# Performance work log

Measured on AMD Instinct MI355X. Metric: run time of the kernel, lower is better.

The kernel has to match this reference:

```python
import jax, jax.numpy as jnp
import numpy as np

D_MODEL = 1024
NHEAD = 16
D_K = D_MODEL // NHEAD


def setup_inputs() -> dict:
    key = jax.random.key(0)
    ks = jax.random.split(key, 8)
    B, S = 2, 2048
    scale = 1.0 / np.sqrt(D_MODEL)
    return {
        "Q": jax.random.normal(ks[0], (B, S, D_MODEL), dtype=jnp.float32),
        "K": jax.random.normal(ks[1], (B, S, D_MODEL), dtype=jnp.float32),
        "V": jax.random.normal(ks[2], (B, S, D_MODEL), dtype=jnp.float32),
        "WQ": jax.random.normal(ks[3], (D_MODEL, D_MODEL), dtype=jnp.float32) * scale,
        "WK": jax.random.normal(ks[4], (D_MODEL, D_MODEL), dtype=jnp.float32) * scale,
        "WV": jax.random.normal(ks[5], (D_MODEL, D_MODEL), dtype=jnp.float32) * scale,
        "Wfc": jax.random.normal(ks[6], (D_MODEL, D_MODEL), dtype=jnp.float32) * scale,
        "bfc": jax.random.normal(ks[7], (D_MODEL,), dtype=jnp.float32) * 0.01,
    }


def reference(Q, K, V, WQ, WK, WV, Wfc, bfc):
    B, Sq, _ = Q.shape
    Skv = K.shape[1]
    # Linear projections (torch Linear: x @ W^T), split into heads: [B, H, S, d_k]
    q = (Q @ WQ.T).reshape(B, Sq, NHEAD, D_K).transpose(0, 2, 1, 3)
    k = (K @ WK.T).reshape(B, Skv, NHEAD, D_K).transpose(0, 2, 1, 3)
    v = (V @ WV.T).reshape(B, Skv, NHEAD, D_K).transpose(0, 2, 1, 3)
    # Scaled dot-product scores: [B, H, Sq, Skv]
    scores = jnp.einsum("bhqd,bhkd->bhqk", q, k) / jnp.sqrt(jnp.float32(D_K))
    # Causal mask (strict upper triangle -> -inf)
    causal = jnp.tril(jnp.ones((Sq, Skv), dtype=bool))
    scores = jnp.where(causal, scores, -jnp.inf)
    attn = jax.nn.softmax(scores, axis=-1)
    y = jnp.einsum("bhqk,bhkd->bhqd", attn, v)
    y = y.transpose(0, 2, 1, 3).reshape(B, Sq, D_MODEL)
    return y @ Wfc.T + bfc
```

## Files before the change

kernel.cpp:

```cpp
#include <hip/hip_runtime.h>

typedef __attribute__((ext_vector_type(8))) short bf16x8;
typedef __attribute__((ext_vector_type(4))) float f32x4;
typedef __attribute__((ext_vector_type(16))) float f32x16;

__device__ __forceinline__ ushort f2bf(float f) {
    union { float f; unsigned u; } x; x.f = f;
    unsigned r = x.u + 0x7fffu + ((x.u >> 16) & 1u);
    return (ushort)(r >> 16);
}

__device__ __forceinline__ void async16(const void* g, void* l) {
    __builtin_amdgcn_global_load_lds(
        (const __attribute__((address_space(1))) void*)g,
        (__attribute__((address_space(3))) void*)l, 16, 0, 0);
}

__device__ __forceinline__ f32x4 mfma16(bf16x8 a, bf16x8 b, f32x4 c) {
    return __builtin_amdgcn_mfma_f32_16x16x32_bf16(a, b, c, 0, 0, 0);
}
__device__ __forceinline__ f32x16 mfma32(bf16x8 a, bf16x8 b, f32x16 c) {
    return __builtin_amdgcn_mfma_f32_32x32x16_bf16(a, b, c, 0, 0, 0);
}

__device__ __forceinline__ f32x4 zero4() { f32x4 z = {0.f, 0.f, 0.f, 0.f}; return z; }

#define PIPE_BARRIER(cond_more)                                          \
    do {                                                                 \
        if (cond_more) asm volatile("s_waitcnt vmcnt(4)" ::: "memory");  \
        else           asm volatile("s_waitcnt vmcnt(0)" ::: "memory");  \
        asm volatile("s_waitcnt lgkmcnt(0)" ::: "memory");               \
        __builtin_amdgcn_sched_barrier(0);                               \
        __builtin_amdgcn_s_barrier();                                    \
        __builtin_amdgcn_sched_barrier(0);                               \
    } while (0)

__global__ void cvt7_kernel(
    const float* __restrict__ s0, const float* __restrict__ s1, const float* __restrict__ s2,
    const float* __restrict__ s3, const float* __restrict__ s4, const float* __restrict__ s5,
    const float* __restrict__ s6,
    ushort* __restrict__ d0, ushort* __restrict__ d1, ushort* __restrict__ d2,
    ushort* __restrict__ d3, ushort* __restrict__ d4, ushort* __restrict__ d5,
    ushort* __restrict__ d6)
{
    int y = blockIdx.y;
    const float* s; ushort* d; int n4;
    if      (y == 0) { s = s0; d = d0; n4 = 1048576; }
    else if (y == 1) { s = s1; d = d1; n4 = 1048576; }
    else if (y == 2) { s = s2; d = d2; n4 = 1048576; }
    else if (y == 3) { s = s3; d = d3; n4 = 262144; }
    else if (y == 4) { s = s4; d = d4; n4 = 262144; }
    else if (y == 5) { s = s5; d = d5; n4 = 262144; }
    else             { s = s6; d = d6; n4 = 262144; }
    int i = blockIdx.x * 256 + threadIdx.x;
    if (i >= n4) return;
    float4 v = ((const float4*)s)[i];
    ushort4 o;
    o.x = f2bf(v.x); o.y = f2bf(v.y); o.z = f2bf(v.z); o.w = f2bf(v.w);
    ((ushort4*)d)[i] = o;
}

template<bool SWAP>
__device__ __forceinline__ void gemm_core(
    const ushort* __restrict__ A, const ushort* __restrict__ W,
    char* smem, int bm, int bn, int tid, f32x4 acc[4][4])
{
    const int lane = tid & 63;
    const int wid  = tid >> 6;
    const int wr = wid >> 1, wc = wid & 1;
    const int l15 = lane & 15, g = lane >> 4;

    auto stage = [&](int kt) {
        char* As = smem + (kt % 3) * 16384;
        char* Bs = As + 8192;
        #pragma unroll
        for (int it = 0; it < 2; ++it) {
            int c = it * 256 + tid;
            int row = c >> 2, inner = c & 3;
            int srcoff = (inner ^ (row & 3)) * 16;
            async16((const char*)A + (size_t)(bm * 128 + row) * 2048 + kt * 64 + srcoff, As + c * 16);
            async16((const char*)W + (size_t)(bn * 128 + row) * 2048 + kt * 64 + srcoff, Bs + c * 16);
        }
    };

    stage(0);
    stage(1);

    for (int kt = 0; kt < 32; ++kt) {
        PIPE_BARRIER(kt < 31);
        if (kt < 30) stage(kt + 2);

        const char* As = smem + (kt % 3) * 16384;
        const char* Bs = As + 8192;
        bf16x8 af[4], bfr[4];
        #pragma unroll
        for (int mt = 0; mt < 4; ++mt) {
            int row = wr * 64 + mt * 16 + l15;
            af[mt] = *(const bf16x8*)(As + ((row * 64 + g * 16) ^ ((row & 3) << 4)));
        }
        #pragma unroll
        for (int nt = 0; nt < 4; ++nt) {
            int row = wc * 64 + nt * 16 + l15;
            bfr[nt] = *(const bf16x8*)(Bs + ((row * 64 + g * 16) ^ ((row & 3) << 4)));
        }
        __builtin_amdgcn_s_setprio(1);
        #pragma unroll
        for (int mt = 0; mt < 4; ++mt)
            #pragma unroll
            for (int nt = 0; nt < 4; ++nt) {
                if (SWAP) acc[mt][nt] = mfma16(bfr[nt], af[mt], acc[mt][nt]);
                else      acc[mt][nt] = mfma16(af[mt], bfr[nt], acc[mt][nt]);
            }
        __builtin_amdgcn_s_setprio(0);
    }
}

__global__ __launch_bounds__(256, 2) void gemm_qkv(
    const ushort* __restrict__ Qb, const ushort* __restrict__ Kb, const ushort* __restrict__ Vb,
    const ushort* __restrict__ WQ, const ushort* __restrict__ WK, const ushort* __restrict__ WV,
    ushort* __restrict__ qhb, ushort* __restrict__ khb, ushort* __restrict__ vhT)
{
    __shared__ __align__(16) char smem[49152];
    const int tid = threadIdx.x;
    const int z  = blockIdx.x % 3;
    const int bm = blockIdx.x / 3;
    const int bn = blockIdx.y;
    const int lane = tid & 63;
    const int wid  = tid >> 6;
    const int wr = wid >> 1, wc = wid & 1;
    const int l15 = lane & 15, g = lane >> 4;

    const ushort* A  = (z == 0) ? Qb : (z == 1) ? Kb : Vb;
    const ushort* Wm = (z == 0) ? WQ : (z == 1) ? WK : WV;

    f32x4 acc[4][4];
    #pragma unroll
    for (int i = 0; i < 4; ++i)
        #pragma unroll
        for (int j = 0; j < 4; ++j) acc[i][j] = zero4();

    if (z == 2) {
        gemm_core<true>(A, Wm, smem, bm, bn, tid, acc);
        #pragma unroll
        for (int mt = 0; mt < 4; ++mt)
            #pragma unroll
            for (int nt = 0; nt < 4; ++nt)
                #pragma unroll
                for (int j = 0; j < 4; ++j) {
                    int n = bn * 128 + wc * 64 + nt * 16 + g * 4 + j;
                    int m = bm * 128 + wr * 64 + mt * 16 + l15;
                    int b = m >> 11, s = m & 2047, h = (n >> 6) & 15, d = n & 63;
                    vhT[(((size_t)(b * 16 + h)) * 64 + d) * 2048 + s] = f2bf(acc[mt][nt][j]);
                }
    } else {
        gemm_core<false>(A, Wm, smem, bm, bn, tid, acc);
        const float scale = (z == 0) ? 0.125f : 1.0f;
        ushort* outb = (z == 0) ? qhb : khb;
        #pragma unroll
        for (int mt = 0; mt < 4; ++mt)
            #pragma unroll
            for (int nt = 0; nt < 4; ++nt)
                #pragma unroll
                for (int j = 0; j < 4; ++j) {
                    int m = bm * 128 + wr * 64 + mt * 16 + g * 4 + j;
                    int n = bn * 128 + wc * 64 + nt * 16 + l15;
                    int b = m >> 11, s = m & 2047, h = n >> 6, d = n & 63;
                    outb[(((size_t)(b * 16 + h)) * 2048 + s) * 64 + d] = f2bf(acc[mt][nt][j] * scale);
                }
    }
}

__global__ __launch_bounds__(256, 2) void gemm_fc(
    const ushort* __restrict__ A, const ushort* __restrict__ W,
    float* __restrict__ outf, const float* __restrict__ bias)
{
    __shared__ __align__(16) char smem[49152];
    const int tid = threadIdx.x;
    const int lane = tid & 63;
    const int wid  = tid >> 6;
    const int wr = wid >> 1, wc = wid & 1;
    const int l15 = lane & 15, g = lane >> 4;

    f32x4 acc[4][4];
    #pragma unroll
    for (int i = 0; i < 4; ++i)
        #pragma unroll
        for (int j = 0; j < 4; ++j) acc[i][j] = zero4();

    gemm_core<false>(A, W, smem, blockIdx.x, blockIdx.y, tid, acc);

    #pragma unroll
    for (int mt = 0; mt < 4; ++mt)
        #pragma unroll
        for (int nt = 0; nt < 4; ++nt)
            #pragma unroll
            for (int j = 0; j < 4; ++j) {
                int m = blockIdx.x * 128 + wr * 64 + mt * 16 + g * 4 + j;
                int n = blockIdx.y * 128 + wc * 64 + nt * 16 + l15;
                outf[(size_t)m * 1024 + n] = acc[mt][nt][j] + bias[n];
            }
}

__global__ __launch_bounds__(512, 2) void attn_kernel(
    const ushort* __restrict__ qh, const ushort* __restrict__ kh,
    const ushort* __restrict__ vhT, ushort* __restrict__ yb)
{
    __shared__ __align__(16) char smem[135168];
    const int tid = threadIdx.x;
    const int lane = tid & 63, wid = tid >> 6;
    const int l31 = lane & 31;
    const int hi  = lane >> 5;
    const int group = wid >> 2;
    const int wq    = wid & 3;
    const int subkv = group * 64;
    const int bh = blockIdx.y;
    const size_t base = (size_t)bh * 2048 * 64;
    const int b_ = bh >> 4, h_ = bh & 15;
    float* oml = (float*)(smem + 98304);

    auto stageK = [&](int t) {
        char* Ks = smem + (t % 3) * 32768;
        #pragma unroll
        for (int it = 0; it < 2; ++it) {
            int c = it * 512 + tid;
            int row = c >> 3, inner = c & 7;
            async16((const char*)kh + (base + (size_t)(t * 128 + row) * 64) * 2 + ((inner ^ (row & 7)) * 16),
                    Ks + c * 16);
        }
    };
    auto stageV = [&](int t) {
        char* Vs = smem + (t % 3) * 32768 + 16384;
        #pragma unroll
        for (int it = 0; it < 2; ++it) {
            int c = it * 512 + tid;
            int row = c >> 4, inner = c & 15;
            async16((const char*)vhT + (base + (size_t)row * 2048 + (size_t)t * 128) * 2 + ((inner ^ (row & 15)) * 16),
                    Vs + c * 16);
        }
    };

    for (int p = 0; p < 2; ++p) {
        const int qt  = (p == 0) ? (int)blockIdx.x : 15 - (int)blockIdx.x;
        const int qrw = qt * 128 + wq * 32;

        bf16x8 qf[4];
        #pragma unroll
        for (int ks = 0; ks < 4; ++ks)
            qf[ks] = *(const bf16x8*)((const char*)qh + (base + (size_t)(qrw + l31) * 64) * 2 + ks * 32 + hi * 16);

        f32x16 o[2];
        #pragma unroll
        for (int r = 0; r < 16; ++r) { o[0][r] = 0.f; o[1][r] = 0.f; }
        float m_run = -1e30f, l_run = 0.f;

        stageK(0); stageV(0);
        if (qt >= 1) { stageK(1); stageV(1); }

        for (int t = 0; t <= qt; ++t) {
            PIPE_BARRIER(t < qt);
            if (t + 2 <= qt) { stageK(t + 2); stageV(t + 2); }

            const int kv0 = t * 128 + subkv;
            if (kv0 <= qrw + 31) {
                const char* Ks = smem + (t % 3) * 32768;
                const char* Vs = Ks + 16384;

                f32x16 st[2];
                #pragma unroll
                for (int r = 0; r < 16; ++r) { st[0][r] = 0.f; st[1][r] = 0.f; }
                __builtin_amdgcn_s_setprio(1);
                #pragma unroll
                for (int tt = 0; tt < 2; ++tt)
                    #pragma unroll
                    for (int ks = 0; ks < 4; ++ks) {
                        int krow = subkv + tt * 32 + l31;
                        int byte = (krow * 128 + ks * 32 + hi * 16) ^ ((krow & 7) << 4);
                        bf16x8 kf = *(const bf16x8*)(Ks + byte);
                        st[tt] = mfma32(kf, qf[ks], st[tt]);
                    }
                __builtin_amdgcn_s_setprio(0);

                if (kv0 + 63 > qrw) {
                    #pragma unroll
                    for (int tt = 0; tt < 2; ++tt)
                        #pragma unroll
                        for (int r = 0; r < 16; ++r) {
                            int kv = kv0 + tt * 32 + (r & 3) + 8 * (r >> 2) + 4 * hi;
                            if (kv > qrw + l31) st[tt][r] = -1e30f;
                        }
                }

                float mx = st[0][0];
                #pragma unroll
                for (int tt = 0; tt < 2; ++tt)
                    #pragma unroll
                    for (int r = 0; r < 16; ++r) mx = fmaxf(mx, st[tt][r]);
                mx = fmaxf(mx, __shfl_xor(mx, 32));

                if (!__all(mx - m_run <= 8.0f)) {
                    float mn = fmaxf(m_run, mx);
                    float corr = __expf(m_run - mn);
                    l_run *= corr;
                    m_run = mn;
                    #pragma unroll
                    for (int r = 0; r < 16; ++r) {
                        int qsrc = (r & 3) + 8 * (r >> 2) + 4 * hi;
                        float c2 = __shfl(corr, qsrc);
                        o[0][r] *= c2; o[1][r] *= c2;
                    }
                }

                float sum = 0.f;
                #pragma unroll
                for (int tt = 0; tt < 2; ++tt)
                    #pragma unroll
                    for (int r = 0; r < 16; ++r) {
                        float pw = __expf(st[tt][r] - m_run);
                        st[tt][r] = pw;
                        sum += pw;
                    }
                sum += __shfl_xor(sum, 32);
                l_run += sum;

                unsigned Wd[2][8], Xw[2][8];
                #pragma unroll
                for (int tt = 0; tt < 2; ++tt)
                    #pragma unroll
                    for (int k = 0; k < 8; ++k) {
                        unsigned w;
                        asm("v_cvt_pk_bf16_f32 %0, %1, %2" : "=v"(w) : "v"(st[tt][2 * k]), "v"(st[tt][2 * k + 1]));
                        Wd[tt][k] = w;
                    }
                #pragma unroll
                for (int tt = 0; tt < 2; ++tt)
                    #pragma unroll
                    for (int k = 0; k < 8; ++k)
                        Xw[tt][k] = __shfl_xor((int)Wd[tt][k], 32);

                #pragma unroll
                for (int ks = 0; ks < 4; ++ks) {
                    const int t2 = ks >> 1, bse = (ks & 1) * 4;
                    unsigned w0 = hi ? Xw[t2][bse + 2] : Wd[t2][bse + 0];
                    unsigned w1 = hi ? Xw[t2][bse + 3] : Wd[t2][bse + 1];
                    unsigned w2 = hi ? Wd[t2][bse + 2] : Xw[t2][bse + 0];
                    unsigned w3 = hi ? Wd[t2][bse + 3] : Xw[t2][bse + 1];
                    unsigned pw4[4] = {w0, w1, w2, w3};
                    bf16x8 pf = *(const bf16x8*)pw4;
                    __builtin_amdgcn_s_setprio(1);
                    #pragma unroll
                    for (int dt = 0; dt < 2; ++dt) {
                        int vrow = dt * 32 + l31;
                        int colB = subkv * 2 + ks * 32 + hi * 16;
                        int byte = vrow * 256 + (colB ^ ((vrow & 15) << 4));
                        bf16x8 vf = *(const bf16x8*)(Vs + byte);
                        o[dt] = mfma32(pf, vf, o[dt]);
                    }
                    __builtin_amdgcn_s_setprio(0);
                }
            }
        }

        __syncthreads();
        if (group == 1) {
            float* pp = oml + (size_t)(wq * 64 + lane) * 36;
            #pragma unroll
            for (int r = 0; r < 16; ++r) { pp[r] = o[0][r]; pp[16 + r] = o[1][r]; }
            pp[32] = m_run; pp[33] = l_run;
        }
        __syncthreads();
        if (group == 0) {
            const float* pp = oml + (size_t)(wq * 64 + lane) * 36;
            float m1 = pp[32], l1 = pp[33];
            float mn = fmaxf(m_run, m1);
            float a0 = __expf(m_run - mn);
            float a1 = __expf(m1 - mn);
            float lt = l_run * a0 + l1 * a1;
            float invl = 1.0f / lt;
            #pragma unroll
            for (int r = 0; r < 16; ++r) {
                int qsrc = (r & 3) + 8 * (r >> 2) + 4 * hi;
                float f0 = __shfl(a0, qsrc);
                float f1 = __shfl(a1, qsrc);
                float iv = __shfl(invl, qsrc);
                float v0 = (o[0][r] * f0 + pp[r] * f1) * iv;
                float v1 = (o[1][r] * f0 + pp[16 + r] * f1) * iv;
                int q = qrw + qsrc;
                size_t rowoff = ((size_t)(b_ * 2048 + q)) * 1024 + h_ * 64;
                yb[rowoff + l31]      = f2bf(v0);
                yb[rowoff + 32 + l31] = f2bf(v1);
            }
        }
        __syncthreads();
    }
}

extern "C" void kernel_launch(void* const* d_in, const int* in_sizes, int n_in,
                              void* d_out, int out_size, void* d_ws, size_t ws_size,
                              hipStream_t stream)
{
    const size_t MD = 4096ull * 1024;
    const size_t WD = 1024ull * 1024;
    ushort* ws  = (ushort*)d_ws;
    ushort* Qb  = ws;
    ushort* Kb  = Qb + MD;
    ushort* Vb  = Kb + MD;
    ushort* qhb = Vb + MD;
    ushort* khb = qhb + MD;
    ushort* vhT = khb + MD;
    ushort* WQb = vhT + MD;
    ushort* WKb = WQb + WD;
    ushort* WVb = WKb + WD;
    ushort* Wfb = WVb + WD;
    ushort* yb  = Qb;

    cvt7_kernel<<<dim3(4096, 7), 256, 0, stream>>>(
        (const float*)d_in[0], (const float*)d_in[1], (const float*)d_in[2],
        (const float*)d_in[3], (const float*)d_in[4], (const float*)d_in[5],
        (const float*)d_in[6],
        Qb, Kb, Vb, WQb, WKb, WVb, Wfb);

    gemm_qkv<<<dim3(96, 8), 256, 0, stream>>>(Qb, Kb, Vb, WQb, WKb, WVb, qhb, khb, vhT);
    attn_kernel<<<dim3(8, 32), 512, 0, stream>>>(qhb, khb, vhT, yb);
    gemm_fc<<<dim3(32, 8), 256, 0, stream>>>(yb, Wfb, (float*)d_out, (const float*)d_in[7]);
}
```

Baseline: 117.0 us.

## Double-buffer attention K/V in smaller LDS, use exp2 with folded log2e scale

Shrinks the attention kernel's LDS from a triple-buffered 132KB to a double-buffered 64KB, reusing the buffer for the cross-group merge, and raises launch bounds so more workgroups can share a CU. The q scale now folds in log2(e) so the softmax can use the native exp2 instruction instead of __expf. It also adds a per-iteration end barrier for buffer reuse and remaps the block index to spread heads across the grid. The trade-offs are a shallower prefetch pipeline and an extra barrier per KV tile; the higher occupancy target may also force register spilling.

```diff
diff --git a/kernel.cpp b/kernel.cpp
--- a/kernel.cpp
+++ b/kernel.cpp
@@ -25,10 +25,25 @@
 
 __device__ __forceinline__ f32x4 zero4() { f32x4 z = {0.f, 0.f, 0.f, 0.f}; return z; }
 
+__device__ __forceinline__ float xhalf_max(float v) {
+    return fmaxf(v, __shfl_xor(v, 32));
+}
+__device__ __forceinline__ float xhalf_sum(float v) {
+    return v + __shfl_xor(v, 32);
+}
+
 #define PIPE_BARRIER(cond_more)                                          \
     do {                                                                 \
         if (cond_more) asm volatile("s_waitcnt vmcnt(4)" ::: "memory");  \
         else           asm volatile("s_waitcnt vmcnt(0)" ::: "memory");  \
+        asm volatile("s_waitcnt lgkmcnt(0)" ::: "memory");               \
+        __builtin_amdgcn_sched_barrier(0);                               \
+        __builtin_amdgcn_s_barrier();                                    \
+        __builtin_amdgcn_sched_barrier(0);                               \
+    } while (0)
+
+#define END_BARRIER()                                                    \
+    do {                                                                 \
         asm volatile("s_waitcnt lgkmcnt(0)" ::: "memory");               \
         __builtin_amdgcn_sched_barrier(0);                               \
         __builtin_amdgcn_s_barrier();                                    \
@@ -154,7 +169,7 @@
                 }
     } else {
         gemm_core<false>(A, Wm, smem, bm, bn, tid, acc);
-        const float scale = (z == 0) ? 0.125f : 1.0f;
+        const float scale = (z == 0) ? 0.18033688011112042f : 1.0f;
         ushort* outb = (z == 0) ? qhb : khb;
         #pragma unroll
         for (int mt = 0; mt < 4; ++mt)
@@ -201,11 +216,11 @@
             }
 }
 
-__global__ __launch_bounds__(512, 2) void attn_kernel(
+__global__ __launch_bounds__(512, 4) void attn_kernel(
     const ushort* __restrict__ qh, const ushort* __restrict__ kh,
     const ushort* __restrict__ vhT, ushort* __restrict__ yb)
 {
-    __shared__ __align__(16) char smem[135168];
+    __shared__ __align__(16) char smem[65536];
     const int tid = threadIdx.x;
     const int lane = tid & 63, wid = tid >> 6;
     const int l31 = lane & 31;
@@ -213,13 +228,15 @@
     const int group = wid >> 2;
     const int wq    = wid & 3;
     const int subkv = group * 64;
-    const int bh = blockIdx.y;
+    const int id = blockIdx.x;
+    const int bh = (id & 7) * 4 + ((id >> 3) & 3);
+    const int qx = id >> 5;
     const size_t base = (size_t)bh * 2048 * 64;
     const int b_ = bh >> 4, h_ = bh & 15;
-    float* oml = (float*)(smem + 98304);
-
-    auto stageK = [&](int t) {
-        char* Ks = smem + (t % 3) * 32768;
+    float* oml = (float*)smem;
+
+    auto stageK = [&](int t, int b) {
+        char* Ks = smem + b * 32768;
         #pragma unroll
         for (int it = 0; it < 2; ++it) {
             int c = it * 512 + tid;
@@ -228,8 +245,8 @@
                     Ks + c * 16);
         }
     };
-    auto stageV = [&](int t) {
-        char* Vs = smem + (t % 3) * 32768 + 16384;
+    auto stageV = [&](int t, int b) {
+        char* Vs = smem + b * 32768 + 16384;
         #pragma unroll
         for (int it = 0; it < 2; ++it) {
             int c = it * 512 + tid;
@@ -240,7 +257,7 @@
     };
 
     for (int p = 0; p < 2; ++p) {
-        const int qt  = (p == 0) ? (int)blockIdx.x : 15 - (int)blockIdx.x;
+        const int qt  = (p == 0) ? qx : 15 - qx;
         const int qrw = qt * 128 + wq * 32;
 
         bf16x8 qf[4];
@@ -253,16 +270,16 @@
         for (int r = 0; r < 16; ++r) { o[0][r] = 0.f; o[1][r] = 0.f; }
         float m_run = -1e30f, l_run = 0.f;
 
-        stageK(0); stageV(0);
-        if (qt >= 1) { stageK(1); stageV(1); }
+        stageK(0, 0); stageV(0, 0);
 
         for (int t = 0; t <= qt; ++t) {
-            PIPE_BARRIER(t < qt);
-            if (t + 2 <= qt) { stageK(t + 2); stageV(t + 2); }
+            const bool more = (t + 1 <= qt);
+            if (more) { stageK(t + 1, (t + 1) & 1); stageV(t + 1, (t + 1) & 1); }
+            PIPE_BARRIER(more);
 
             const int kv0 = t * 128 + subkv;
             if (kv0 <= qrw + 31) {
-                const char* Ks = smem + (t % 3) * 32768;
+                const char* Ks = smem + (t & 1) * 32768;
                 const char* Vs = Ks + 16384;
 
                 f32x16 st[2];
@@ -295,11 +312,11 @@
                 for (int tt = 0; tt < 2; ++tt)
                     #pragma unroll
                     for (int r = 0; r < 16; ++r) mx = fmaxf(mx, st[tt][r]);
-                mx = fmaxf(mx, __shfl_xor(mx, 32));
+                mx = xhalf_max(mx);
 
                 if (!__all(mx - m_run <= 8.0f)) {
                     float mn = fmaxf(m_run, mx);
-                    float corr = __expf(m_run - mn);
+                    float corr = __builtin_amdgcn_exp2f(m_run - mn);
                     l_run *= corr;
                     m_run = mn;
                     #pragma unroll
@@ -315,11 +332,11 @@
                 for (int tt = 0; tt < 2; ++tt)
                     #pragma unroll
                     for (int r = 0; r < 16; ++r) {
-                        float pw = __expf(st[tt][r] - m_run);
+                        float pw = __builtin_amdgcn_exp2f(st[tt][r] - m_run);
                         st[tt][r] = pw;
                         sum += pw;
                     }
-                sum += __shfl_xor(sum, 32);
+                sum = xhalf_sum(sum);
                 l_run += sum;
 
                 unsigned Wd[2][8], Xw[2][8];
@@ -358,9 +375,9 @@
                     __builtin_amdgcn_s_setprio(0);
                 }
             }
-        }
-
-        __syncthreads();
+            END_BARRIER();
+        }
+
         if (group == 1) {
             float* pp = oml + (size_t)(wq * 64 + lane) * 36;
             #pragma unroll
@@ -372,8 +389,8 @@
             const float* pp = oml + (size_t)(wq * 64 + lane) * 36;
             float m1 = pp[32], l1 = pp[33];
             float mn = fmaxf(m_run, m1);
-            float a0 = __expf(m_run - mn);
-            float a1 = __expf(m1 - mn);
+            float a0 = __builtin_amdgcn_exp2f(m_run - mn);
+            float a1 = __builtin_amdgcn_exp2f(m1 - mn);
             float lt = l_run * a0 + l1 * a1;
             float invl = 1.0f / lt;
             #pragma unroll
@@ -420,6 +437,6 @@
         Qb, Kb, Vb, WQb, WKb, WVb, Wfb);
 
     gemm_qkv<<<dim3(96, 8), 256, 0, stream>>>(Qb, Kb, Vb, WQb, WKb, WVb, qhb, khb, vhT);
-    attn_kernel<<<dim3(8, 32), 512, 0, stream>>>(qhb, khb, vhT, yb);
+    attn_kernel<<<256, 512, 0, stream>>>(qhb, khb, vhT, yb);
     gemm_fc<<<dim3(32, 8), 256, 0, stream>>>(yb, Wfb, (float*)d_out, (const float*)d_in[7]);
 }
```

New measurement: 116.8 us. About the same (-0.1%).
